# Kernel optimization log

Measured on AMD Instinct MI355X. Metric: run time of the kernel, lower is better.

The kernel has to match this reference:

```python
import jax, jax.numpy as jnp
import numpy as np

N_HEAD = 16


def setup_inputs() -> dict:
    key = jax.random.key(0)
    ks = jax.random.split(key, 9)
    b, s, d = 4, 2048, 1024
    scale = 1.0 / np.sqrt(d)
    return {
        "x": jax.random.normal(ks[0], (b, s, d), dtype=jnp.float32),
        "Wq": jax.random.normal(ks[1], (d, d), dtype=jnp.float32) * scale,
        "bq": jax.random.normal(ks[2], (d,), dtype=jnp.float32) * 0.01,
        "Wk": jax.random.normal(ks[3], (d, d), dtype=jnp.float32) * scale,
        "bk": jax.random.normal(ks[4], (d,), dtype=jnp.float32) * 0.01,
        "Wv": jax.random.normal(ks[5], (d, d), dtype=jnp.float32) * scale,
        "bv": jax.random.normal(ks[6], (d,), dtype=jnp.float32) * 0.01,
        "Wo": jax.random.normal(ks[7], (d, d), dtype=jnp.float32) * scale,
        "bo": jax.random.normal(ks[8], (d,), dtype=jnp.float32) * 0.01,
        "mask": 1,
    }


def reference(x, Wq, bq, Wk, bk, Wv, bv, Wo, bo, mask):
    b, s, d = x.shape
    h = N_HEAD
    dh = d // h
    # projections -> [b, h, s, dh]
    def proj(W, bias):
        return (x @ W + bias).reshape(b, s, h, dh).transpose(0, 2, 1, 3)

    Q = proj(Wq, bq)
    K = proj(Wk, bk)
    V = proj(Wv, bv)

    # full S x S scores (module materializes them explicitly)
    scores = jnp.einsum('bhqd,bhkd->bhqk', Q, K)
    if mask:
        causal = jnp.triu(jnp.ones((s, s), dtype=bool), k=1)
        scores = jnp.where(causal, -jnp.inf, scores)
    scores = scores / jnp.sqrt(jnp.asarray(dh, dtype=scores.dtype))
    attn = jax.nn.softmax(scores, axis=-1)
    out = jnp.einsum('bhqk,bhkd->bhqd', attn, V)  # [b, h, s, dh]
    out = out.transpose(0, 2, 1, 3).reshape(b, s, d)
    return out @ Wo + bo
```

## Files before the change

kernel.cpp:

```cpp
#include <hip/hip_runtime.h>

typedef unsigned short u16;
typedef unsigned int u32;
typedef __bf16 bf16x4 __attribute__((ext_vector_type(4)));
typedef __bf16 bf16x8 __attribute__((ext_vector_type(8)));
typedef float f32x4 __attribute__((ext_vector_type(4)));
typedef float f32x16 __attribute__((ext_vector_type(16)));

#define BATCH 4
#define SLEN 2048
#define DMODEL 1024
#define NHEAD 16
#define DHEAD 64
#define MROWS (BATCH * SLEN)

__device__ __forceinline__ u16 f32_to_bf16(float f) {
  u32 u = __float_as_uint(f);
  u32 r = (u + 0x7FFFu + ((u >> 16) & 1u)) >> 16;
  return (u16)r;
}
__device__ __forceinline__ u32 pack_bf16x2(float a, float b) {
  return (u32)f32_to_bf16(a) | ((u32)f32_to_bf16(b) << 16);
}

__device__ __forceinline__ u32 pack_trunc(float lo, float hi) {
#if __has_builtin(__builtin_amdgcn_perm)
  return __builtin_amdgcn_perm(__float_as_uint(hi), __float_as_uint(lo), 0x07060302u);
#else
  return (__float_as_uint(hi) & 0xFFFF0000u) | (__float_as_uint(lo) >> 16);
#endif
}
__device__ __forceinline__ u32 pack_round(float lo, float hi) {
  u32 ul = __float_as_uint(lo) + 0x8000u;
  u32 uh = __float_as_uint(hi) + 0x8000u;
#if __has_builtin(__builtin_amdgcn_perm)
  return __builtin_amdgcn_perm(uh, ul, 0x07060302u);
#else
  return (uh & 0xFFFF0000u) | (ul >> 16);
#endif
}

#if __has_builtin(__builtin_amdgcn_exp2f)
#define EXP2(x) __builtin_amdgcn_exp2f(x)
#else
#define EXP2(x) exp2f(x)
#endif

typedef const __attribute__((address_space(1))) void* gas_cv;
typedef __attribute__((address_space(3))) void* las_v;
__device__ __forceinline__ void async16(const u16* g, u16* l) {
  __builtin_amdgcn_global_load_lds((gas_cv)g, (las_v)l, 16, 0, 0);
}


__global__ void convert_x_kernel(const float* __restrict__ x, u16* __restrict__ xb) {
  size_t i = ((size_t)blockIdx.x * 256 + threadIdx.x) * 8;
  float4 v0 = *(const float4*)(x + i);
  float4 v1 = *(const float4*)(x + i + 4);
  uint4 o;
  o.x = pack_bf16x2(v0.x, v0.y);
  o.y = pack_bf16x2(v0.z, v0.w);
  o.z = pack_bf16x2(v1.x, v1.y);
  o.w = pack_bf16x2(v1.z, v1.w);
  *(uint4*)(xb + i) = o;
}

__global__ void transpose_w_kernel(const float* __restrict__ Wq, const float* __restrict__ Wk,
                                   const float* __restrict__ Wv, const float* __restrict__ Wo,
                                   u16* __restrict__ wqkvt, u16* __restrict__ wot) {
  __shared__ float tile[32][33];
  int z = blockIdx.z;
  const float* src = (z == 0) ? Wq : (z == 1) ? Wk : (z == 2) ? Wv : Wo;
  u16* dst = (z < 3) ? (wqkvt + (size_t)z * DMODEL * DMODEL) : wot;
  int c0 = blockIdx.x * 32, r0 = blockIdx.y * 32;
  int tx = threadIdx.x & 31, ty = threadIdx.x >> 5;
#pragma unroll
  for (int i = 0; i < 4; ++i)
    tile[ty + 8 * i][tx] = src[(size_t)(r0 + ty + 8 * i) * DMODEL + c0 + tx];
  __syncthreads();
#pragma unroll
  for (int i = 0; i < 4; ++i)
    dst[(size_t)(c0 + ty + 8 * i) * DMODEL + r0 + tx] = f32_to_bf16(tile[tx][ty + 8 * i]);
}

__global__ void concat_bias_kernel(const float* __restrict__ bq, const float* __restrict__ bk,
                                   const float* __restrict__ bv, float* __restrict__ bqkv) {
  int i = blockIdx.x * 256 + threadIdx.x;
  float v = (i < 1024) ? bq[i] : (i < 2048) ? bk[i - 1024] : bv[i - 2048];
  bqkv[i] = v;
}

__global__ void transpose_v_kernel(const u16* __restrict__ qkv, u16* __restrict__ vt) {
  __shared__ u16 tile[32][33];
  const int bh = blockIdx.z;
  const int b = bh >> 4, h = bh & 15;
  const int s0 = blockIdx.x * 32, d0 = blockIdx.y * 32;
  const int tx = threadIdx.x & 31, ty = threadIdx.x >> 5;
#pragma unroll
  for (int i = 0; i < 4; ++i)
    tile[ty + 8 * i][tx] =
        qkv[(size_t)(b * SLEN + s0 + ty + 8 * i) * (3 * DMODEL) + 2 * DMODEL + h * DHEAD + d0 + tx];
  __syncthreads();
#pragma unroll
  for (int i = 0; i < 4; ++i)
    vt[(size_t)(bh * DHEAD + d0 + ty + 8 * i) * SLEN + s0 + tx] = tile[tx][ty + 8 * i];
}

template <int OUT_BF16>
__global__ __launch_bounds__(256) void gemm_bt_kernel(const u16* __restrict__ A,
                                                      const u16* __restrict__ Bt,
                                                      const float* __restrict__ bias,
                                                      void* __restrict__ Cout,
                                                      int M, int N, int K) {
  __shared__ u16 sA[128 * 32];
  __shared__ u16 sB[128 * 32];
  const int tid = threadIdx.x;
  const int wv = tid >> 6, lane = tid & 63;
  const int wr = wv >> 1, wc = wv & 1;
  const int col = lane & 15, quad = lane >> 4;
  const int m0 = blockIdx.x * 128;
  const int n0 = blockIdx.y * 128;

  f32x4 acc[4][4] = {};

  const int lr = tid >> 2;
  const int ls = tid & 3;
  const size_t a_base = (size_t)(m0 + lr) * K + ls * 8;
  const size_t b_base = (size_t)(n0 + lr) * K + ls * 8;
  u16* ldsA0 = sA + ((tid >> 6) << 9);
  u16* ldsA1 = ldsA0 + 2048;
  u16* ldsB0 = sB + ((tid >> 6) << 9);
  u16* ldsB1 = ldsB0 + 2048;

  for (int k0 = 0; k0 < K; k0 += 32) {
    async16(A + a_base + k0, ldsA0);
    async16(A + a_base + (size_t)64 * K + k0, ldsA1);
    async16(Bt + b_base + k0, ldsB0);
    async16(Bt + b_base + (size_t)64 * K + k0, ldsB1);
    __syncthreads();
    bf16x8 af[4], bfr[4];
#pragma unroll
    for (int i = 0; i < 4; ++i)
      af[i] = *(const bf16x8*)(sA + (wr * 64 + i * 16 + col) * 32 + quad * 8);
#pragma unroll
    for (int j = 0; j < 4; ++j)
      bfr[j] = *(const bf16x8*)(sB + (wc * 64 + j * 16 + col) * 32 + quad * 8);
#pragma unroll
    for (int i = 0; i < 4; ++i)
#pragma unroll
      for (int j = 0; j < 4; ++j)
        acc[i][j] = __builtin_amdgcn_mfma_f32_16x16x32_bf16(af[i], bfr[j], acc[i][j], 0, 0, 0);
    __syncthreads();
  }

#pragma unroll
  for (int i = 0; i < 4; ++i) {
#pragma unroll
    for (int j = 0; j < 4; ++j) {
      int n = n0 + wc * 64 + j * 16 + col;
      float bia = bias[n];
#pragma unroll
      for (int r = 0; r < 4; ++r) {
        int m = m0 + wr * 64 + i * 16 + quad * 4 + r;
        float v = acc[i][j][r] + bia;
        if (OUT_BF16)
          ((u16*)Cout)[(size_t)m * N + n] = f32_to_bf16(v);
        else
          ((float*)Cout)[(size_t)m * N + n] = v;
      }
    }
  }
}

__global__ __launch_bounds__(256, 2) void attn_kernel(const u16* __restrict__ qkv,
                                                      const u16* __restrict__ vt,
                                                      u16* __restrict__ out) {
  const int bh = blockIdx.y;
  const int b = bh >> 4, h = bh & 15;
  const int tid = threadIdx.x;
  const int wv = tid >> 6, lane = tid & 63;
  const int c = lane & 31, hi = lane >> 5;
  const int bx = blockIdx.x;
  const int sfirst = bx * 4 + wv;

  __shared__ u16 sK[2][64 * 64];
  __shared__ u16 sV[2][64 * 64];

  const u16* kbase = qkv + ((size_t)(b * SLEN)) * (3 * DMODEL) + DMODEL + h * DHEAD;
  const u16* vbase = vt + ((size_t)bh * DHEAD) * SLEN;
  const float scl2 = 0.125f * 1.44269504088896f;

  const int lrow = lane >> 3;
  const int sga = (lane & 7) ^ lrow;
  const int r0a = wv * 16, r0b = wv * 16 + 8;
  const int cs = c & 7;

  for (int half = 0; half < 2; ++half) {
    const int s2 = half ? (63 - sfirst) : sfirst;
    const int qbase = s2 * 32;
    const int nt_own = s2 / 2 + 1;
    const int nt = half ? (32 - 2 * bx) : (2 * bx + 2);

    const u16* qrow =
        qkv + ((size_t)(b * SLEN + qbase + c)) * (3 * DMODEL) + h * DHEAD + hi * 8;
    bf16x8 aQ[4];
#pragma unroll
    for (int ks = 0; ks < 4; ++ks) aQ[ks] = *(const bf16x8*)(qrow + ks * 16);

    f32x16 accO[2] = {};
    float m2 = -1e30f, l_i = 0.0f;

    async16(kbase + (size_t)(r0a + lrow) * (3 * DMODEL) + sga * 8, sK[0] + r0a * 64);
    async16(kbase + (size_t)(r0b + lrow) * (3 * DMODEL) + sga * 8, sK[0] + r0b * 64);
    async16(vbase + (size_t)(r0a + lrow) * SLEN + sga * 8, sV[0] + r0a * 64);
    async16(vbase + (size_t)(r0b + lrow) * SLEN + sga * 8, sV[0] + r0b * 64);

    for (int t = 0; t < nt; ++t) {
      const int kv0 = t * 64;
      const int cur = t & 1, nxt = cur ^ 1;

      if (t + 1 < nt) {
        const int kvn = kv0 + 64;
        async16(kbase + (size_t)(kvn + r0a + lrow) * (3 * DMODEL) + sga * 8, sK[nxt] + r0a * 64);
        async16(kbase + (size_t)(kvn + r0b + lrow) * (3 * DMODEL) + sga * 8, sK[nxt] + r0b * 64);
        async16(vbase + (size_t)(r0a + lrow) * SLEN + kvn + sga * 8, sV[nxt] + r0a * 64);
        async16(vbase + (size_t)(r0b + lrow) * SLEN + kvn + sga * 8, sV[nxt] + r0b * 64);
        asm volatile("s_waitcnt vmcnt(4)");
      } else {
        asm volatile("s_waitcnt vmcnt(0)");
      }
      __builtin_amdgcn_sched_barrier(0);
      __builtin_amdgcn_s_barrier();
      __builtin_amdgcn_sched_barrier(0);

      if (t < nt_own) {
        const u16* sKc = sK[cur];
        const u16* sVc = sV[cur];
        bf16x8 bK[2][4], bV[2][4];
#pragma unroll
        for (int m = 0; m < 2; ++m) {
          const int rb = (m * 32 + c) * 64;
#pragma unroll
          for (int ks = 0; ks < 4; ++ks) {
            bK[m][ks] = *(const bf16x8*)(sKc + rb + (((ks * 2 + hi) ^ cs) << 3));
            bf16x4 vlo = *(const bf16x4*)(sVc + rb + (((ks * 2) ^ cs) << 3) + 4 * hi);
            bf16x4 vhi = *(const bf16x4*)(sVc + rb + (((ks * 2 + 1) ^ cs) << 3) + 4 * hi);
            bV[m][ks] = __builtin_shufflevector(vlo, vhi, 0, 1, 2, 3, 4, 5, 6, 7);
          }
        }

        f32x16 accST[2] = {};
#pragma unroll
        for (int ks = 0; ks < 4; ++ks)
#pragma unroll
          for (int m = 0; m < 2; ++m)
            accST[m] = __builtin_amdgcn_mfma_f32_32x32x16_bf16(bK[m][ks], aQ[ks],
                                                               accST[m], 0, 0, 0);

        if (t == nt_own - 1) {
          const int q = qbase + c;
          const int kvh = kv0 + 4 * hi;
#pragma unroll
          for (int m = 0; m < 2; ++m)
#pragma unroll
            for (int r = 0; r < 16; ++r) {
              int kv = kvh + m * 32 + ((r & 3) + 8 * (r >> 2));
              if (kv > q) accST[m][r] = -1e30f;
            }
        }

        float h0 = fmaxf(fmaxf(accST[0][0], accST[0][1]), fmaxf(accST[0][2], accST[0][3]));
        float h1 = fmaxf(fmaxf(accST[0][4], accST[0][5]), fmaxf(accST[0][6], accST[0][7]));
        float h2 = fmaxf(fmaxf(accST[0][8], accST[0][9]), fmaxf(accST[0][10], accST[0][11]));
        float h3 = fmaxf(fmaxf(accST[0][12], accST[0][13]), fmaxf(accST[0][14], accST[0][15]));
        float h4 = fmaxf(fmaxf(accST[1][0], accST[1][1]), fmaxf(accST[1][2], accST[1][3]));
        float h5 = fmaxf(fmaxf(accST[1][4], accST[1][5]), fmaxf(accST[1][6], accST[1][7]));
        float h6 = fmaxf(fmaxf(accST[1][8], accST[1][9]), fmaxf(accST[1][10], accST[1][11]));
        float h7 = fmaxf(fmaxf(accST[1][12], accST[1][13]), fmaxf(accST[1][14], accST[1][15]));
        float rmax = fmaxf(fmaxf(fmaxf(h0, h1), fmaxf(h2, h3)),
                           fmaxf(fmaxf(h4, h5), fmaxf(h6, h7)));
        rmax = fmaxf(rmax, __shfl_xor(rmax, 32));
        float rmaxs = rmax * scl2;
        const bool noresc = __all(rmaxs <= m2);
        float mnew = noresc ? m2 : fmaxf(m2, rmaxs);
        float alpha = noresc ? 1.0f : EXP2(m2 - mnew);
        m2 = mnew;

        float s0 = 0.f, s1 = 0.f, s2s = 0.f, s3 = 0.f;
#pragma unroll
        for (int m = 0; m < 2; ++m) {
#pragma unroll
          for (int r = 0; r < 16; r += 4) {
            float p0 = EXP2(__builtin_fmaf(accST[m][r + 0], scl2, -mnew));
            float p1 = EXP2(__builtin_fmaf(accST[m][r + 1], scl2, -mnew));
            float p2 = EXP2(__builtin_fmaf(accST[m][r + 2], scl2, -mnew));
            float p3 = EXP2(__builtin_fmaf(accST[m][r + 3], scl2, -mnew));
            accST[m][r + 0] = p0;
            accST[m][r + 1] = p1;
            accST[m][r + 2] = p2;
            accST[m][r + 3] = p3;
            s0 += p0;
            s1 += p1;
            s2s += p2;
            s3 += p3;
          }
        }
        float sacc = (s0 + s1) + (s2s + s3);
        sacc += __shfl_xor(sacc, 32);
        if (noresc) {
          l_i += sacc;
        } else {
          l_i = l_i * alpha + sacc;
#pragma unroll
          for (int m = 0; m < 2; ++m)
#pragma unroll
            for (int r = 0; r < 16; ++r) accO[m][r] *= alpha;
        }

        bf16x8 aP[4];
#pragma unroll
        for (int m = 0; m < 2; ++m)
#pragma unroll
          for (int s = 0; s < 2; ++s) {
            union {
              uint4 u;
              bf16x8 v;
            } cvt;
            cvt.u.x = pack_trunc(accST[m][8 * s + 0], accST[m][8 * s + 1]);
            cvt.u.y = pack_trunc(accST[m][8 * s + 2], accST[m][8 * s + 3]);
            cvt.u.z = pack_trunc(accST[m][8 * s + 4], accST[m][8 * s + 5]);
            cvt.u.w = pack_trunc(accST[m][8 * s + 6], accST[m][8 * s + 7]);
            aP[m * 2 + s] = cvt.v;
          }

#pragma unroll
        for (int ks = 0; ks < 4; ++ks)
#pragma unroll
          for (int m = 0; m < 2; ++m)
            accO[m] = __builtin_amdgcn_mfma_f32_32x32x16_bf16(bV[m][ks], aP[ks],
                                                              accO[m], 0, 0, 0);
      }

      __builtin_amdgcn_sched_barrier(0);
      __builtin_amdgcn_s_barrier();
      __builtin_amdgcn_sched_barrier(0);
    }

    {
      float rl = 1.0f / l_i;
      size_t rowoff =
          ((size_t)(b * SLEN + qbase + c)) * DMODEL + h * DHEAD + 4 * hi;
#pragma unroll
      for (int m = 0; m < 2; ++m)
#pragma unroll
        for (int j = 0; j < 4; ++j) {
          uint2 pk;
          pk.x = pack_round(accO[m][4 * j + 0] * rl, accO[m][4 * j + 1] * rl);
          pk.y = pack_round(accO[m][4 * j + 2] * rl, accO[m][4 * j + 3] * rl);
          *(uint2*)(out + rowoff + m * 32 + 8 * j) = pk;
        }
    }
  }
}


extern "C" void kernel_launch(void* const* d_in, const int* in_sizes, int n_in,
                              void* d_out, int out_size, void* d_ws, size_t ws_size,
                              hipStream_t stream) {
  const float* x = (const float*)d_in[0];
  const float* Wq = (const float*)d_in[1];
  const float* bq = (const float*)d_in[2];
  const float* Wk = (const float*)d_in[3];
  const float* bk = (const float*)d_in[4];
  const float* Wv = (const float*)d_in[5];
  const float* bv = (const float*)d_in[6];
  const float* Wo = (const float*)d_in[7];
  const float* bo = (const float*)d_in[8];

  char* ws = (char*)d_ws;
  u16* xb = (u16*)ws;
  u16* wqkvt = (u16*)(ws + ((size_t)16 << 20));
  u16* wot = (u16*)(ws + ((size_t)22 << 20));
  u16* qkv = (u16*)(ws + ((size_t)24 << 20));
  u16* attnO = (u16*)(ws + ((size_t)72 << 20));
  float* bqkv = (float*)(ws + ((size_t)88 << 20));
  u16* vtp = xb;

  convert_x_kernel<<<4096, 256, 0, stream>>>(x, xb);
  transpose_w_kernel<<<dim3(32, 32, 4), 256, 0, stream>>>(Wq, Wk, Wv, Wo, wqkvt, wot);
  concat_bias_kernel<<<12, 256, 0, stream>>>(bq, bk, bv, bqkv);
  gemm_bt_kernel<1><<<dim3(64, 24), 256, 0, stream>>>(xb, wqkvt, bqkv, (void*)qkv,
                                                      MROWS, 3 * DMODEL, DMODEL);
  transpose_v_kernel<<<dim3(64, 2, 64), 256, 0, stream>>>(qkv, vtp);
  attn_kernel<<<dim3(8, BATCH * NHEAD), 256, 0, stream>>>(qkv, vtp, attnO);
  gemm_bt_kernel<0><<<dim3(64, 8), 256, 0, stream>>>(attnO, wot, bo, d_out,
                                                     MROWS, DMODEL, DMODEL);
}
```

Measured before the change: 286.0 us.

## Fuse V transpose into QKV GEMM epilogue and raise MFMA wave priority

The QKV projection GEMM now writes V directly in transposed per-head layout from its epilogue, while Q and K go to a compact 2*DMODEL-stride buffer. This removes the separate transpose_v kernel launch and its extra read and write of V. The attention kernel now uses the narrower row stride for Q/K and wraps its MFMA blocks in s_setprio to favour matrix issue. The transposed V stores are 8-byte writes strided by SLEN, which may coalesce worse than the row-major stores they replace.

```diff
diff --git a/kernel.cpp b/kernel.cpp
--- a/kernel.cpp
+++ b/kernel.cpp
@@ -90,27 +90,12 @@
   bqkv[i] = v;
 }
 
-__global__ void transpose_v_kernel(const u16* __restrict__ qkv, u16* __restrict__ vt) {
-  __shared__ u16 tile[32][33];
-  const int bh = blockIdx.z;
-  const int b = bh >> 4, h = bh & 15;
-  const int s0 = blockIdx.x * 32, d0 = blockIdx.y * 32;
-  const int tx = threadIdx.x & 31, ty = threadIdx.x >> 5;
-#pragma unroll
-  for (int i = 0; i < 4; ++i)
-    tile[ty + 8 * i][tx] =
-        qkv[(size_t)(b * SLEN + s0 + ty + 8 * i) * (3 * DMODEL) + 2 * DMODEL + h * DHEAD + d0 + tx];
-  __syncthreads();
-#pragma unroll
-  for (int i = 0; i < 4; ++i)
-    vt[(size_t)(bh * DHEAD + d0 + ty + 8 * i) * SLEN + s0 + tx] = tile[tx][ty + 8 * i];
-}
-
-template <int OUT_BF16>
+template <int OUT_BF16, int FUSE_V>
 __global__ __launch_bounds__(256) void gemm_bt_kernel(const u16* __restrict__ A,
                                                       const u16* __restrict__ Bt,
                                                       const float* __restrict__ bias,
                                                       void* __restrict__ Cout,
+                                                      u16* __restrict__ vtout,
                                                       int M, int N, int K) {
   __shared__ u16 sA[128 * 32];
   __shared__ u16 sB[128 * 32];
@@ -159,20 +144,31 @@
     for (int j = 0; j < 4; ++j) {
       int n = n0 + wc * 64 + j * 16 + col;
       float bia = bias[n];
-#pragma unroll
-      for (int r = 0; r < 4; ++r) {
-        int m = m0 + wr * 64 + i * 16 + quad * 4 + r;
-        float v = acc[i][j][r] + bia;
-        if (OUT_BF16)
-          ((u16*)Cout)[(size_t)m * N + n] = f32_to_bf16(v);
-        else
-          ((float*)Cout)[(size_t)m * N + n] = v;
+      if (FUSE_V && n >= 2 * DMODEL) {
+        const int hh = (n - 2 * DMODEL) >> 6, dh = n & 63;
+        const int mb = m0 + wr * 64 + i * 16 + quad * 4;
+        const int bb = mb >> 11, s0 = mb & 2047;
+        uint2 pk;
+        pk.x = pack_bf16x2(acc[i][j][0] + bia, acc[i][j][1] + bia);
+        pk.y = pack_bf16x2(acc[i][j][2] + bia, acc[i][j][3] + bia);
+        *(uint2*)(vtout + ((size_t)((bb * 16 + hh) * 64 + dh)) * SLEN + s0) = pk;
+      } else {
+        const int cstride = FUSE_V ? (2 * DMODEL) : N;
+#pragma unroll
+        for (int r = 0; r < 4; ++r) {
+          int m = m0 + wr * 64 + i * 16 + quad * 4 + r;
+          float v = acc[i][j][r] + bia;
+          if (OUT_BF16)
+            ((u16*)Cout)[(size_t)m * cstride + n] = f32_to_bf16(v);
+          else
+            ((float*)Cout)[(size_t)m * cstride + n] = v;
+        }
       }
     }
   }
 }
 
-__global__ __launch_bounds__(256, 2) void attn_kernel(const u16* __restrict__ qkv,
+__global__ __launch_bounds__(256, 2) void attn_kernel(const u16* __restrict__ qk,
                                                       const u16* __restrict__ vt,
                                                       u16* __restrict__ out) {
   const int bh = blockIdx.y;
@@ -186,7 +182,7 @@
   __shared__ u16 sK[2][64 * 64];
   __shared__ u16 sV[2][64 * 64];
 
-  const u16* kbase = qkv + ((size_t)(b * SLEN)) * (3 * DMODEL) + DMODEL + h * DHEAD;
+  const u16* kbase = qk + ((size_t)(b * SLEN)) * (2 * DMODEL) + DMODEL + h * DHEAD;
   const u16* vbase = vt + ((size_t)bh * DHEAD) * SLEN;
   const float scl2 = 0.125f * 1.44269504088896f;
 
@@ -202,7 +198,7 @@
     const int nt = half ? (32 - 2 * bx) : (2 * bx + 2);
 
     const u16* qrow =
-        qkv + ((size_t)(b * SLEN + qbase + c)) * (3 * DMODEL) + h * DHEAD + hi * 8;
+        qk + ((size_t)(b * SLEN + qbase + c)) * (2 * DMODEL) + h * DHEAD + hi * 8;
     bf16x8 aQ[4];
 #pragma unroll
     for (int ks = 0; ks < 4; ++ks) aQ[ks] = *(const bf16x8*)(qrow + ks * 16);
@@ -210,8 +206,8 @@
     f32x16 accO[2] = {};
     float m2 = -1e30f, l_i = 0.0f;
 
-    async16(kbase + (size_t)(r0a + lrow) * (3 * DMODEL) + sga * 8, sK[0] + r0a * 64);
-    async16(kbase + (size_t)(r0b + lrow) * (3 * DMODEL) + sga * 8, sK[0] + r0b * 64);
+    async16(kbase + (size_t)(r0a + lrow) * (2 * DMODEL) + sga * 8, sK[0] + r0a * 64);
+    async16(kbase + (size_t)(r0b + lrow) * (2 * DMODEL) + sga * 8, sK[0] + r0b * 64);
     async16(vbase + (size_t)(r0a + lrow) * SLEN + sga * 8, sV[0] + r0a * 64);
     async16(vbase + (size_t)(r0b + lrow) * SLEN + sga * 8, sV[0] + r0b * 64);
 
@@ -221,8 +217,8 @@
 
       if (t + 1 < nt) {
         const int kvn = kv0 + 64;
-        async16(kbase + (size_t)(kvn + r0a + lrow) * (3 * DMODEL) + sga * 8, sK[nxt] + r0a * 64);
-        async16(kbase + (size_t)(kvn + r0b + lrow) * (3 * DMODEL) + sga * 8, sK[nxt] + r0b * 64);
+        async16(kbase + (size_t)(kvn + r0a + lrow) * (2 * DMODEL) + sga * 8, sK[nxt] + r0a * 64);
+        async16(kbase + (size_t)(kvn + r0b + lrow) * (2 * DMODEL) + sga * 8, sK[nxt] + r0b * 64);
         async16(vbase + (size_t)(r0a + lrow) * SLEN + kvn + sga * 8, sV[nxt] + r0a * 64);
         async16(vbase + (size_t)(r0b + lrow) * SLEN + kvn + sga * 8, sV[nxt] + r0b * 64);
         asm volatile("s_waitcnt vmcnt(4)");
@@ -250,12 +246,14 @@
         }
 
         f32x16 accST[2] = {};
+        __builtin_amdgcn_s_setprio(1);
 #pragma unroll
         for (int ks = 0; ks < 4; ++ks)
 #pragma unroll
           for (int m = 0; m < 2; ++m)
             accST[m] = __builtin_amdgcn_mfma_f32_32x32x16_bf16(bK[m][ks], aQ[ks],
                                                                accST[m], 0, 0, 0);
+        __builtin_amdgcn_s_setprio(0);
 
         if (t == nt_own - 1) {
           const int q = qbase + c;
@@ -333,12 +331,14 @@
             aP[m * 2 + s] = cvt.v;
           }
 
+        __builtin_amdgcn_s_setprio(1);
 #pragma unroll
         for (int ks = 0; ks < 4; ++ks)
 #pragma unroll
           for (int m = 0; m < 2; ++m)
             accO[m] = __builtin_amdgcn_mfma_f32_32x32x16_bf16(bV[m][ks], aP[ks],
                                                               accO[m], 0, 0, 0);
+        __builtin_amdgcn_s_setprio(0);
       }
 
       __builtin_amdgcn_sched_barrier(0);
@@ -381,18 +381,17 @@
   u16* xb = (u16*)ws;
   u16* wqkvt = (u16*)(ws + ((size_t)16 << 20));
   u16* wot = (u16*)(ws + ((size_t)22 << 20));
-  u16* qkv = (u16*)(ws + ((size_t)24 << 20));
+  u16* qk = (u16*)(ws + ((size_t)24 << 20));
+  u16* vtp = (u16*)(ws + ((size_t)56 << 20));
   u16* attnO = (u16*)(ws + ((size_t)72 << 20));
   float* bqkv = (float*)(ws + ((size_t)88 << 20));
-  u16* vtp = xb;
 
   convert_x_kernel<<<4096, 256, 0, stream>>>(x, xb);
   transpose_w_kernel<<<dim3(32, 32, 4), 256, 0, stream>>>(Wq, Wk, Wv, Wo, wqkvt, wot);
   concat_bias_kernel<<<12, 256, 0, stream>>>(bq, bk, bv, bqkv);
-  gemm_bt_kernel<1><<<dim3(64, 24), 256, 0, stream>>>(xb, wqkvt, bqkv, (void*)qkv,
-                                                      MROWS, 3 * DMODEL, DMODEL);
-  transpose_v_kernel<<<dim3(64, 2, 64), 256, 0, stream>>>(qkv, vtp);
-  attn_kernel<<<dim3(8, BATCH * NHEAD), 256, 0, stream>>>(qkv, vtp, attnO);
-  gemm_bt_kernel<0><<<dim3(64, 8), 256, 0, stream>>>(attnO, wot, bo, d_out,
-                                                     MROWS, DMODEL, DMODEL);
-}
+  gemm_bt_kernel<1, 1><<<dim3(64, 24), 256, 0, stream>>>(xb, wqkvt, bqkv, (void*)qk, vtp,
+                                                         MROWS, 3 * DMODEL, DMODEL);
+  attn_kernel<<<dim3(8, BATCH * NHEAD), 256, 0, stream>>>(qk, vtp, attnO);
+  gemm_bt_kernel<0, 0><<<dim3(64, 8), 256, 0, stream>>>(attnO, wot, bo, d_out, nullptr,
+                                                        MROWS, DMODEL, DMODEL);
+}
```

Measured after the change: 280.4 us. 1.02x faster.
